# Performance work log

Hardware: AMD Instinct MI355X
Metric: run time of the kernel (lower is better)

## Reference

```python
import jax, jax.numpy as jnp
import numpy as np

EMBED_DIM = 512
PATCH = 16
QUANT_N = 1024
QUANT_DIM = 256
LN_EPS = 1e-5


def setup_inputs() -> dict:
    key = jax.random.key(0)
    k1, k2, k3, k4 = jax.random.split(key, 4)
    B, T, M = 16, 8192, 128
    fbank = jax.random.normal(k1, (B, T, M), dtype=jnp.float32)
    # xavier-normal conv weight (O,I,kH,kW), frozen in the original module
    fan = PATCH * PATCH + EMBED_DIM
    conv_w = jax.random.normal(k2, (EMBED_DIM, 1, PATCH, PATCH), dtype=jnp.float32) * np.sqrt(2.0 / fan)
    proj = jax.random.normal(k3, (EMBED_DIM, QUANT_DIM), dtype=jnp.float32) * np.sqrt(2.0 / (EMBED_DIM + QUANT_DIM))
    codebook = jax.random.normal(k4, (QUANT_N, QUANT_DIM), dtype=jnp.float32)
    return {"fbank": fbank, "conv_w": conv_w, "proj": proj, "codebook": codebook}


def _l2norm(x, eps=1e-12):
    return x / jnp.maximum(jnp.linalg.norm(x, axis=-1, keepdims=True), eps)


def reference(fbank, conv_w, proj, codebook):
    # patch embedding: Conv2d(1, D, k=16, s=16) over (B, 1, T, mel)
    x = fbank[:, None, :, :]  # B,1,T,M
    feats = jax.lax.conv_general_dilated(
        x, conv_w, window_strides=(PATCH, PATCH), padding='VALID',
        dimension_numbers=('NCHW', 'OIHW', 'NCHW'))  # B,D,T/16,M/16
    B, D, H, W = feats.shape
    feats = feats.reshape(B, D, H * W).transpose(0, 2, 1)  # B,N,D
    # LayerNorm without affine
    mu = jnp.mean(feats, axis=-1, keepdims=True)
    var = jnp.var(feats, axis=-1, keepdims=True)
    feats = (feats - mu) * jax.lax.rsqrt(var + LN_EPS)
    # random projection quantizer: l2norm(x @ P) vs l2-normalized codebook;
    # argmin euclidean distance == argmax cosine similarity for unit vectors
    p = _l2norm(jnp.einsum('bnd,dq->bnq', feats, proj))  # B,N,Q
    cb = _l2norm(codebook)                                # K,Q
    sim = jnp.einsum('bnq,kq->bnk', p, cb)                # B,N,K
    embed_ind = jnp.argmax(sim, axis=-1)                  # B,N int
    return embed_ind
```

## Files before the change

kernel.cpp:

```cpp
#include <hip/hip_runtime.h>
#include <math.h>

#define QD 256
#define QN 1024
#define TT 8192

typedef __bf16 bf16x8 __attribute__((ext_vector_type(8)));
typedef float  f32x16 __attribute__((ext_vector_type(16)));
typedef unsigned short ushort_t;
typedef unsigned short us8 __attribute__((ext_vector_type(8)));

#define PL  0
#define WS_ 49152
#define P1_ 50176
#define MU_ 51200
#define LM_ 53248
#define TN_ 53376
#define LX_ 54400
#define TH_ 55424
#define CN_ 55552
#define CC_ 55680
#define SMEM_TOTAL 59776

__device__ __forceinline__ void split3(float x, ushort_t& h, ushort_t& m, ushort_t& l) {
    unsigned int xu = __float_as_uint(x);
    h = (ushort_t)(xu >> 16);
    float hf = __uint_as_float(xu & 0xFFFF0000u);
    float r1 = x - hf;
    unsigned int r1u = __float_as_uint(r1);
    m = (ushort_t)(r1u >> 16);
    float mf = __uint_as_float(r1u & 0xFFFF0000u);
    float r2 = r1 - mf;
    l = (ushort_t)(__float_as_uint(r2) >> 16);
}
__device__ __forceinline__ f32x16 MF(bf16x8 a, bf16x8 b, f32x16 c) {
    return __builtin_amdgcn_mfma_f32_32x32x16_bf16(a, b, c, 0, 0, 0);
}

__global__ __launch_bounds__(256) void k_pre(const float* __restrict__ convw,
                                             const float* __restrict__ proj,
                                             const float* __restrict__ cb,
                                             ushort_t* __restrict__ cbph,
                                             float* __restrict__ cbn,
                                             ushort_t* __restrict__ w2p,
                                             float* __restrict__ wsum,
                                             float* __restrict__ p1) {
    int bx = blockIdx.x, t = threadIdx.x;
    if (bx < 256) {
        int c = bx*4 + (t>>6), lane = t&63;
        float4 v = ((const float4*)(cb + (size_t)c*QD))[lane];
        float ss = v.x*v.x + v.y*v.y + v.z*v.z + v.w*v.w;
        #pragma unroll
        for (int off = 32; off > 0; off >>= 1) ss += __shfl_down(ss, off);
        ss = __shfl(ss, 0);
        float inv = 1.0f/fmaxf(sqrtf(ss), 1e-12f);
        float4 vn = make_float4(v.x*inv, v.y*inv, v.z*inv, v.w*inv);
        *(float4*)(cbn + (size_t)c*QD + 4*lane) = vn;
        float vals[4] = {vn.x, vn.y, vn.z, vn.w};
        #pragma unroll
        for (int i = 0; i < 4; ++i) {
            int k = 4*lane + i;
            size_t base = ((size_t)(k>>4)*32 + (c>>5))*512 + (((k>>3)&1)*32 + (c&31))*8 + (k&7);
            cbph[base] = (ushort_t)(__float_as_uint(vals[i]) >> 16);
        }
    } else if (bx < 320) {
        int col0 = (bx - 256) * 4;
        __shared__ float4 colv4[512];
        const float* src = proj + col0;
        colv4[t]       = *(const float4*)(src + (size_t)t * 256);
        colv4[t + 256] = *(const float4*)(src + (size_t)(t + 256) * 256);
        __syncthreads();
        float a0 = 0.f, a1 = 0.f, a2 = 0.f, a3 = 0.f;
        #pragma unroll 16
        for (int d = 0; d < 512; ++d) {
            float wv = convw[d*256 + t];
            float4 cv = colv4[d];
            a0 += wv*cv.x; a1 += wv*cv.y; a2 += wv*cv.z; a3 += wv*cv.w;
        }
        float accs[4] = {a0, a1, a2, a3};
        #pragma unroll
        for (int j = 0; j < 4; ++j) {
            int col = col0 + j;
            ushort_t hb, mb, lb; split3(accs[j], hb, mb, lb);
            size_t base = ((size_t)(t>>4)*8 + (col>>5))*512 + (((t>>3)&1)*32 + (col&31))*8 + (t&7);
            w2p[base] = hb;
            w2p[base + 65536] = mb;
            w2p[base + 131072] = lb;
        }
    } else if (bx == 320) {
        float s = 0.f;
        #pragma unroll 32
        for (int d = 0; d < 512; ++d) s += convw[d*256 + t];
        wsum[t] = s;
    } else {
        float s = 0.f;
        #pragma unroll 32
        for (int d = 0; d < 512; ++d) s += proj[d*256 + t];
        p1[t] = s;
    }
}

__global__ __launch_bounds__(512, 4) void k_mega(const float* __restrict__ fbank,
                                                 const ushort_t* __restrict__ w2p,
                                                 const ushort_t* __restrict__ cbph,
                                                 const float* __restrict__ cbn,
                                                 const float* __restrict__ wsum,
                                                 const float* __restrict__ p1,
                                                 int* __restrict__ out) {
    __shared__ char smem[SMEM_TOTAL];
    float* wsS   = (float*)(smem + WS_);
    float* p1S   = (float*)(smem + P1_);
    float* muS   = (float*)(smem + MU_);
    float* lnMuS = (float*)(smem + LM_);
    float* tn2P  = (float*)(smem + TN_);
    float* lmaxS = (float*)(smem + LX_);
    float* thrS  = (float*)(smem + TH_);
    int*   cntS  = (int*)(smem + CN_);
    ushort_t* candS = (ushort_t*)(smem + CC_);

    int tid = threadIdx.x;
    int n0 = blockIdx.x * 32;
    int w = tid >> 6, lane = tid & 63;
    int n31 = lane & 31, h = lane >> 5;
    size_t loff = (size_t)lane * 16;
    const char* w2pc = (const char*)w2p;
    const char* cbhc = (const char*)cbph;

    auto loadB1 = [&](int kcv, bf16x8 (&dst)[3]) {
        #pragma unroll
        for (int q = 0; q < 3; ++q)
            dst[q] = *(const bf16x8*)(w2pc + (size_t)q*131072 + (size_t)(kcv*8 + w)*1024 + loff);
    };
    auto loadB2s = [&](int sw, int kcv, bf16x8 (&dst)[2]) {
        dst[0] = *(const bf16x8*)(cbhc + (size_t)(kcv*32 + 16*sw + w    )*1024 + loff);
        dst[1] = *(const bf16x8*)(cbhc + (size_t)(kcv*32 + 16*sw + w + 8)*1024 + loff);
    };
    auto loadA = [&](int kcv, bf16x8 (&a)[3]) {
        #pragma unroll
        for (int p = 0; p < 3; ++p)
            a[p] = *(const bf16x8*)(smem + p*16384 + kcv*1024 + loff);
    };
    auto compute6 = [&](bf16x8 (&a)[3], bf16x8 (&b)[3], f32x16& acc) {
        acc = MF(a[0], b[0], acc);
        acc = MF(a[0], b[1], acc);
        acc = MF(a[1], b[0], acc);
        acc = MF(a[1], b[1], acc);
        acc = MF(a[0], b[2], acc);
        acc = MF(a[2], b[0], acc);
    };

    float4 va[2], vb[2];
    #pragma unroll
    for (int i = 0; i < 2; ++i) {
        int id = tid + 512*i;
        int kc = id >> 6, cl = id & 63;
        int tok = cl & 31, hh2 = cl >> 5;
        int n = n0 + tok;
        int b = n >> 12, r = n & 4095, th = r >> 3, wm = r & 7;
        const float* src = fbank + ((size_t)(b*TT + th*16 + kc))*128 + wm*16 + hh2*8;
        va[i] = ((const float4*)src)[0];
        vb[i] = ((const float4*)src)[1];
    }
    if (tid < 256) wsS[tid] = wsum[tid];
    else           p1S[tid - 256] = p1[tid - 256];
    __syncthreads();

    float mupart = 0.f;
    #pragma unroll
    for (int i = 0; i < 2; ++i) {
        int id = tid + 512*i;
        int kc = id >> 6, cl = id & 63;
        int hh2 = cl >> 5;
        float vals[8] = {va[i].x, va[i].y, va[i].z, va[i].w, vb[i].x, vb[i].y, vb[i].z, vb[i].w};
        us8 hv, mv, lv;
        #pragma unroll
        for (int j = 0; j < 8; ++j) {
            ushort_t a_, b_, c_; split3(vals[j], a_, b_, c_);
            hv[j] = a_; mv[j] = b_; lv[j] = c_;
            mupart += vals[j] * wsS[16*kc + 8*hh2 + j];
        }
        char* cp = smem + kc*1024 + cl*16;
        *(us8*)cp = hv;
        *(us8*)(cp + 16384) = mv;
        *(us8*)(cp + 32768) = lv;
    }

    bf16x8 bA[3], bB[3];
    loadB1(0, bA);

    muS[(tid>>5)*32 + (tid&31)] = mupart;
    __syncthreads();

    if (tid < 32) {
        float pm = 0.f;
        #pragma unroll
        for (int s = 0; s < 16; ++s) pm += muS[s*32 + tid];
        lnMuS[tid] = pm * (1.f/512.f);
    }

    f32x16 accE, accO;
    #pragma unroll
    for (int r2 = 0; r2 < 16; ++r2) { accE[r2] = 0.f; accO[r2] = 0.f; }
    for (int kc = 0; kc < 16; kc += 2) {
        loadB1(kc + 1, bB);
        { bf16x8 a[3]; loadA(kc, a); compute6(a, bA, accE); }
        if (kc + 2 < 16) loadB1(kc + 2, bA);
        { bf16x8 a[3]; loadA(kc + 1, a); compute6(a, bB, accO); }
    }

    bf16x8 qA[2], qB[2];
    loadB2s(0, 0, qA);

    __syncthreads();

    {
        int q = 32*w + n31;
        float p1v = p1S[q];
        #pragma unroll
        for (int reg = 0; reg < 16; ++reg) {
            int tok = (reg&3) + 8*(reg>>2) + 4*h;
            float tv = (accE[reg] + accO[reg]) - lnMuS[tok]*p1v;
            *(float*)(smem + 16384 + tok*1024 + q*4) = tv;
            *(ushort_t*)(smem + (q>>4)*1024 + (((q>>3)&1)*32 + tok)*16 + (q&7)*2)
                = (ushort_t)(__float_as_uint(tv) >> 16);
            float sq2 = tv*tv;
            #pragma unroll
            for (int msk = 1; msk < 32; msk <<= 1) sq2 += __shfl_xor(sq2, msk);
            if (n31 == 0) tn2P[tok*8 + w] = sq2;
        }
    }
    __syncthreads();

    #pragma unroll
    for (int sw = 0; sw < 2; ++sw) {
        f32x16 s0, s1;
        #pragma unroll
        for (int r2 = 0; r2 < 16; ++r2) { s0[r2] = 0.f; s1[r2] = 0.f; }
        for (int kc = 0; kc < 16; kc += 2) {
            loadB2s(sw, kc + 1, qB);
            {
                bf16x8 ah = *(const bf16x8*)(smem + kc*1024 + loff);
                s0 = MF(ah, qA[0], s0); s1 = MF(ah, qA[1], s1);
            }
            if (kc + 2 < 16) loadB2s(sw, kc + 2, qA);
            else if (sw == 0) loadB2s(1, 0, qA);
            {
                bf16x8 ah = *(const bf16x8*)(smem + (kc+1)*1024 + loff);
                s0 = MF(ah, qB[0], s0); s1 = MF(ah, qB[1], s1);
            }
        }
        #pragma unroll
        for (int reg = 0; reg < 16; ++reg) {
            int tok = (reg&3) + 8*(reg>>2) + 4*h;
            float m = fmaxf(s0[reg], s1[reg]);
            #pragma unroll
            for (int msk = 1; msk < 32; msk <<= 1) m = fmaxf(m, __shfl_xor(m, msk));
            if (n31 == 0) lmaxS[tok*8 + w] = (sw == 0) ? m : fmaxf(lmaxS[tok*8 + w], m);
        }
        __syncthreads();
        if (tid < 32) {
            float g = -3.4e38f, sq = 0.f;
            #pragma unroll
            for (int p = 0; p < 8; ++p) { g = fmaxf(g, lmaxS[tid*8 + p]); sq += tn2P[tid*8 + p]; }
            thrS[tid] = g - 0.04f*sqrtf(sq);
            if (sw == 0) cntS[tid] = 0;
        }
        __syncthreads();
        #pragma unroll
        for (int reg = 0; reg < 16; ++reg) {
            int tok = (reg&3) + 8*(reg>>2) + 4*h;
            float th_ = thrS[tok];
            if (s0[reg] >= th_) { int p = atomicAdd(&cntS[tok], 1); if (p < 64) candS[tok*64 + p] = (ushort_t)(512*sw + 32*w + n31); }
            if (s1[reg] >= th_) { int p = atomicAdd(&cntS[tok], 1); if (p < 64) candS[tok*64 + p] = (ushort_t)(512*sw + 32*(w + 8) + n31); }
        }
    }
    __syncthreads();

    int grp = lane >> 2, sub = lane & 3;
    #pragma unroll 1
    for (int tk = 0; tk < 4; ++tk) {
        int tok = 4*w + tk;
        int cnt = cntS[tok];
        bool full = (cnt > 64);
        int nc = full ? 1024 : cnt;
        const float4* tp = (const float4*)(smem + 16384 + (size_t)tok*1024 + (size_t)sub*256);
        float bv = -3.4e38f; int bi = 0x7fffffff;
        #pragma unroll 1
        for (int base = 0; base < nc; base += 16) {
            int ci = base + grp;
            int code = 0x7fffffff;
            float part = 0.f;
            if (ci < nc) {
                code = full ? ci : (int)candS[tok*64 + ci];
                const float4* cp = (const float4*)(cbn + (size_t)code*256 + (size_t)sub*64);
                float a0 = 0.f, a1 = 0.f, a2 = 0.f, a3 = 0.f;
                #pragma unroll
                for (int j = 0; j < 16; j += 4) {
                    float4 c0 = cp[j], c1 = cp[j+1], c2 = cp[j+2], c3 = cp[j+3];
                    float4 t0 = tp[j], t1 = tp[j+1], t2 = tp[j+2], t3 = tp[j+3];
                    a0 += c0.x*t0.x + c0.y*t0.y + c0.z*t0.z + c0.w*t0.w;
                    a1 += c1.x*t1.x + c1.y*t1.y + c1.z*t1.z + c1.w*t1.w;
                    a2 += c2.x*t2.x + c2.y*t2.y + c2.z*t2.z + c2.w*t2.w;
                    a3 += c3.x*t3.x + c3.y*t3.y + c3.z*t3.z + c3.w*t3.w;
                }
                part = (a0 + a1) + (a2 + a3);
            }
            float d = part;
            d += __shfl_xor(d, 1);
            d += __shfl_xor(d, 2);
            if (ci >= nc) d = -3.4e38f;
            #pragma unroll
            for (int msk = 4; msk < 64; msk <<= 1) {
                float od = __shfl_xor(d, msk);
                int   oc = __shfl_xor(code, msk);
                if (od > d || (od == d && oc < code)) { d = od; code = oc; }
            }
            if (d > bv || (d == bv && code < bi)) { bv = d; bi = code; }
        }
        if (lane == 0) out[n0 + tok] = bi;
    }
}

extern "C" void kernel_launch(void* const* d_in, const int* in_sizes, int n_in,
                              void* d_out, int out_size, void* d_ws, size_t ws_size,
                              hipStream_t stream) {
    const float* fbank = (const float*)d_in[0];
    const float* convw = (const float*)d_in[1];
    const float* proj  = (const float*)d_in[2];
    const float* cbook = (const float*)d_in[3];
    int* out = (int*)d_out;

    char* ws = (char*)d_ws;
    ushort_t* cbph = (ushort_t*)ws;
    float* cbn     = (float*)(ws + 0x080000);
    ushort_t* w2p  = (ushort_t*)(ws + 0x180000);
    float* wsum    = (float*)(ws + 0x1E0000);
    float* p1      = (float*)(ws + 0x1E1000);

    hipLaunchKernelGGL(k_pre,  dim3(322),  dim3(256), 0, stream,
                       convw, proj, cbook, cbph, cbn, w2p, wsum, p1);
    hipLaunchKernelGGL(k_mega, dim3(2048), dim3(512), 0, stream,
                       fbank, w2p, cbph, cbn, wsum, p1, out);
}
```

Measured before the change: 330.1 us.

## Replace per-wave reduction arrays with shared atomics and drop staging barriers

Loads the wsum and p1 values straight from global memory into registers instead of staging them through shared memory, which removes one barrier. The per-token norm sum and max similarity now use shared-memory atomics (atomicAdd, and atomicMax on an order-preserving float encoding), replacing the per-wave partial arrays and the serial single-warp reduction step along with its barrier. It also pre-reduces the mean partials with a lane shuffle, lowers the candidate capacity from 64 to 48 to shrink LDS, and interleaves the rescoring float4 loads so lanes read adjacent addresses. The price is atomic contention, plus a higher chance that a token overflows the smaller candidate list and falls back to the full 1024-code scan.

New measurement: 301.3 us. 1.1x faster.

```diff
diff --git a/kernel.cpp b/kernel.cpp
--- a/kernel.cpp
+++ b/kernel.cpp
@@ -11,16 +11,14 @@
 typedef unsigned short us8 __attribute__((ext_vector_type(8)));
 
 #define PL  0
-#define WS_ 49152
-#define P1_ 50176
-#define MU_ 51200
-#define LM_ 53248
-#define TN_ 53376
-#define LX_ 54400
-#define TH_ 55424
-#define CN_ 55552
-#define CC_ 55680
-#define SMEM_TOTAL 59776
+#define MU_ 49152
+#define LM_ 50176
+#define T2_ 50304
+#define TR_ 50432
+#define CN_ 50560
+#define CC_ 50688
+#define SMEM_TOTAL 53760
+#define CCAP 48
 
 __device__ __forceinline__ void split3(float x, ushort_t& h, ushort_t& m, ushort_t& l) {
     unsigned int xu = __float_as_uint(x);
@@ -35,6 +33,13 @@
 }
 __device__ __forceinline__ f32x16 MF(bf16x8 a, bf16x8 b, f32x16 c) {
     return __builtin_amdgcn_mfma_f32_32x32x16_bf16(a, b, c, 0, 0, 0);
+}
+__device__ __forceinline__ unsigned fenc(float f) {
+    unsigned u = __float_as_uint(f);
+    return (u & 0x80000000u) ? ~u : (u | 0x80000000u);
+}
+__device__ __forceinline__ float fdec(unsigned u) {
+    return (u & 0x80000000u) ? __uint_as_float(u ^ 0x80000000u) : __uint_as_float(~u);
 }
 
 __global__ __launch_bounds__(256) void k_pre(const float* __restrict__ convw,
@@ -108,14 +113,11 @@
                                                  const float* __restrict__ p1,
                                                  int* __restrict__ out) {
     __shared__ char smem[SMEM_TOTAL];
-    float* wsS   = (float*)(smem + WS_);
-    float* p1S   = (float*)(smem + P1_);
-    float* muS   = (float*)(smem + MU_);
-    float* lnMuS = (float*)(smem + LM_);
-    float* tn2P  = (float*)(smem + TN_);
-    float* lmaxS = (float*)(smem + LX_);
-    float* thrS  = (float*)(smem + TH_);
-    int*   cntS  = (int*)(smem + CN_);
+    float*    muS   = (float*)(smem + MU_);
+    float*    lnMuS = (float*)(smem + LM_);
+    float*    tn2A  = (float*)(smem + T2_);
+    unsigned* thrR  = (unsigned*)(smem + TR_);
+    int*      cntS  = (int*)(smem + CN_);
     ushort_t* candS = (ushort_t*)(smem + CC_);
 
     int tid = threadIdx.x;
@@ -161,23 +163,32 @@
         va[i] = ((const float4*)src)[0];
         vb[i] = ((const float4*)src)[1];
     }
-    if (tid < 256) wsS[tid] = wsum[tid];
-    else           p1S[tid - 256] = p1[tid - 256];
-    __syncthreads();
+    int wb0 = 16*(tid >> 6) + 8*((tid >> 5) & 1);
+    float4 w00 = *(const float4*)(wsum + wb0);
+    float4 w01 = *(const float4*)(wsum + wb0 + 4);
+    float4 w10 = *(const float4*)(wsum + wb0 + 128);
+    float4 w11 = *(const float4*)(wsum + wb0 + 132);
+
+    if (tid < 32) { tn2A[tid] = 0.f; thrR[tid] = 0u; cntS[tid] = 0; }
+
+    float wsv[2][8];
+    wsv[0][0]=w00.x; wsv[0][1]=w00.y; wsv[0][2]=w00.z; wsv[0][3]=w00.w;
+    wsv[0][4]=w01.x; wsv[0][5]=w01.y; wsv[0][6]=w01.z; wsv[0][7]=w01.w;
+    wsv[1][0]=w10.x; wsv[1][1]=w10.y; wsv[1][2]=w10.z; wsv[1][3]=w10.w;
+    wsv[1][4]=w11.x; wsv[1][5]=w11.y; wsv[1][6]=w11.z; wsv[1][7]=w11.w;
 
     float mupart = 0.f;
     #pragma unroll
     for (int i = 0; i < 2; ++i) {
         int id = tid + 512*i;
         int kc = id >> 6, cl = id & 63;
-        int hh2 = cl >> 5;
         float vals[8] = {va[i].x, va[i].y, va[i].z, va[i].w, vb[i].x, vb[i].y, vb[i].z, vb[i].w};
         us8 hv, mv, lv;
         #pragma unroll
         for (int j = 0; j < 8; ++j) {
             ushort_t a_, b_, c_; split3(vals[j], a_, b_, c_);
             hv[j] = a_; mv[j] = b_; lv[j] = c_;
-            mupart += vals[j] * wsS[16*kc + 8*hh2 + j];
+            mupart += vals[j] * wsv[i][j];
         }
         char* cp = smem + kc*1024 + cl*16;
         *(us8*)cp = hv;
@@ -188,13 +199,14 @@
     bf16x8 bA[3], bB[3];
     loadB1(0, bA);
 
-    muS[(tid>>5)*32 + (tid&31)] = mupart;
+    float mu2 = mupart + __shfl_xor(mupart, 32);
+    if (lane < 32) muS[w*32 + lane] = mu2;
     __syncthreads();
 
     if (tid < 32) {
         float pm = 0.f;
         #pragma unroll
-        for (int s = 0; s < 16; ++s) pm += muS[s*32 + tid];
+        for (int s = 0; s < 8; ++s) pm += muS[s*32 + tid];
         lnMuS[tid] = pm * (1.f/512.f);
     }
 
@@ -208,6 +220,7 @@
         { bf16x8 a[3]; loadA(kc + 1, a); compute6(a, bB, accO); }
     }
 
+    float p1v = p1[32*w + n31];
     bf16x8 qA[2], qB[2];
     loadB2s(0, 0, qA);
 
@@ -215,7 +228,6 @@
 
     {
         int q = 32*w + n31;
-        float p1v = p1S[q];
         #pragma unroll
         for (int reg = 0; reg < 16; ++reg) {
             int tok = (reg&3) + 8*(reg>>2) + 4*h;
@@ -226,7 +238,7 @@
             float sq2 = tv*tv;
             #pragma unroll
             for (int msk = 1; msk < 32; msk <<= 1) sq2 += __shfl_xor(sq2, msk);
-            if (n31 == 0) tn2P[tok*8 + w] = sq2;
+            if (n31 == 0) atomicAdd(&tn2A[tok], sq2);
         }
     }
     __syncthreads();
@@ -255,23 +267,15 @@
             float m = fmaxf(s0[reg], s1[reg]);
             #pragma unroll
             for (int msk = 1; msk < 32; msk <<= 1) m = fmaxf(m, __shfl_xor(m, msk));
-            if (n31 == 0) lmaxS[tok*8 + w] = (sw == 0) ? m : fmaxf(lmaxS[tok*8 + w], m);
-        }
-        __syncthreads();
-        if (tid < 32) {
-            float g = -3.4e38f, sq = 0.f;
-            #pragma unroll
-            for (int p = 0; p < 8; ++p) { g = fmaxf(g, lmaxS[tid*8 + p]); sq += tn2P[tid*8 + p]; }
-            thrS[tid] = g - 0.04f*sqrtf(sq);
-            if (sw == 0) cntS[tid] = 0;
+            if (n31 == 0) atomicMax(&thrR[tok], fenc(m));
         }
         __syncthreads();
         #pragma unroll
         for (int reg = 0; reg < 16; ++reg) {
             int tok = (reg&3) + 8*(reg>>2) + 4*h;
-            float th_ = thrS[tok];
-            if (s0[reg] >= th_) { int p = atomicAdd(&cntS[tok], 1); if (p < 64) candS[tok*64 + p] = (ushort_t)(512*sw + 32*w + n31); }
-            if (s1[reg] >= th_) { int p = atomicAdd(&cntS[tok], 1); if (p < 64) candS[tok*64 + p] = (ushort_t)(512*sw + 32*(w + 8) + n31); }
+            float th_ = fdec(thrR[tok]) - 0.04f*sqrtf(tn2A[tok]);
+            if (s0[reg] >= th_) { int p = atomicAdd(&cntS[tok], 1); if (p < CCAP) candS[tok*CCAP + p] = (ushort_t)(512*sw + 32*w + n31); }
+            if (s1[reg] >= th_) { int p = atomicAdd(&cntS[tok], 1); if (p < CCAP) candS[tok*CCAP + p] = (ushort_t)(512*sw + 32*(w + 8) + n31); }
         }
     }
     __syncthreads();
@@ -281,9 +285,9 @@
     for (int tk = 0; tk < 4; ++tk) {
         int tok = 4*w + tk;
         int cnt = cntS[tok];
-        bool full = (cnt > 64);
+        bool full = (cnt > CCAP);
         int nc = full ? 1024 : cnt;
-        const float4* tp = (const float4*)(smem + 16384 + (size_t)tok*1024 + (size_t)sub*256);
+        const float4* tp4 = (const float4*)(smem + 16384 + (size_t)tok*1024);
         float bv = -3.4e38f; int bi = 0x7fffffff;
         #pragma unroll 1
         for (int base = 0; base < nc; base += 16) {
@@ -291,13 +295,15 @@
             int code = 0x7fffffff;
             float part = 0.f;
             if (ci < nc) {
-                code = full ? ci : (int)candS[tok*64 + ci];
-                const float4* cp = (const float4*)(cbn + (size_t)code*256 + (size_t)sub*64);
+                code = full ? ci : (int)candS[tok*CCAP + ci];
+                const float4* cp4 = (const float4*)(cbn + (size_t)code*256);
                 float a0 = 0.f, a1 = 0.f, a2 = 0.f, a3 = 0.f;
                 #pragma unroll
-                for (int j = 0; j < 16; j += 4) {
-                    float4 c0 = cp[j], c1 = cp[j+1], c2 = cp[j+2], c3 = cp[j+3];
-                    float4 t0 = tp[j], t1 = tp[j+1], t2 = tp[j+2], t3 = tp[j+3];
+                for (int jj = 0; jj < 16; jj += 4) {
+                    float4 c0 = cp4[(jj  )*4 + sub], t0 = tp4[(jj  )*4 + sub];
+                    float4 c1 = cp4[(jj+1)*4 + sub], t1 = tp4[(jj+1)*4 + sub];
+                    float4 c2 = cp4[(jj+2)*4 + sub], t2 = tp4[(jj+2)*4 + sub];
+                    float4 c3 = cp4[(jj+3)*4 + sub], t3 = tp4[(jj+3)*4 + sub];
                     a0 += c0.x*t0.x + c0.y*t0.y + c0.z*t0.z + c0.w*t0.w;
                     a1 += c1.x*t1.x + c1.y*t1.y + c1.z*t1.z + c1.w*t1.w;
                     a2 += c2.x*t2.x + c2.y*t2.y + c2.z*t2.z + c2.w*t2.w;
```
